# Optimization experiments

Measured on AMD Instinct MI355X. Metric: run time of the kernel, lower is better.

## Reference

```python
import jax, jax.numpy as jnp
import numpy as np

B, T, D = 4, 2048, 1024
H, K, V, S, C = 8, 128, 128, 512, 256
R = T // C
W = 2 * C
TAU = float(K) ** 0.5
NEG = 1e30  # INFTY_APPROX from source


def rel_shift(x):
    # Transformer-XL relative shift; x: [B,H,R,C,W]
    lead = x.shape[:-2]
    c, w = x.shape[-2:]
    x = jnp.pad(x, [(0, 0)] * (x.ndim - 1) + [(1, 0)])
    x = x.reshape(*lead, w + 1, c)
    return x[..., 1:, :].reshape(*lead, c, w)


def setup_inputs():
    key = jax.random.key(0)
    ks = jax.random.split(key, 9)
    sd = lambda n: 1.0 / np.sqrt(n)
    f32 = jnp.float32
    return dict(
        x=jax.random.normal(ks[0], (B, T, D), f32),
        g_ln=jnp.ones((D,), f32),
        Wq=jax.random.normal(ks[1], (D, H, K), f32) * sd(D),
        Wk=jax.random.normal(ks[2], (D, H, K), f32) * sd(D),
        Wv=jax.random.normal(ks[3], (D, H, V), f32) * sd(D),
        codebook=jax.random.normal(ks[4], (H, S, K), f32),
        xl_r=jax.random.normal(ks[5], (H, W, K), f32) * sd(D),
        xl_u=jax.random.normal(ks[6], (H, K), f32) * 0.02,
        xl_v=jax.random.normal(ks[7], (H, K), f32) * 0.02,
        Wo=jax.random.normal(ks[8], (H, V, D), f32) * sd(H * V),
    )


def reference(x, g_ln, Wq, Wk, Wv, codebook, xl_r, xl_u, xl_v, Wo):
    # RMSNorm
    xt = x * jax.lax.rsqrt(jnp.mean(jnp.square(x), axis=-1, keepdims=True) + 1e-6) * g_ln
    # QKV projections, reshaped to blocks: [B,H,R,C,*]
    q = jnp.einsum('btd,dhk->bhtk', xt, Wq).reshape(B, H, R, C, K)
    k = jnp.einsum('btd,dhk->bhtk', xt, Wk).reshape(B, H, R, C, K)
    v = jnp.einsum('btd,dhv->bhtv', xt, Wv).reshape(B, H, R, C, V)
    # VQ codebook assignment (per-head nearest codeword)
    d2 = (jnp.sum(k * k, -1, keepdims=True)
          - 2.0 * jnp.einsum('bhrck,hsk->bhrcs', k, codebook)
          + jnp.sum(codebook * codebook, -1)[None, :, None, None, :])
    z = jnp.argmin(d2, axis=-1)                      # shortcodes [B,H,R,C]
    delta = jax.nn.one_hot(z, S, dtype=k.dtype)      # [B,H,R,C,S]
    k_hat_q = jnp.einsum('bhrcs,hsk->bhrck', delta, codebook)
    k_hat = k + jax.lax.stop_gradient(k_hat_q - k)   # straight-through quantized keys
    # causal cumulative per-code cluster stats ('matmul' reduction from source)
    d1 = jnp.sum(delta, axis=3)                      # counts per block [B,H,R,S]
    d1c = jnp.cumsum(d1, axis=2)
    fracs = jnp.tril(jnp.einsum('bhrs,bhgs->bhsrg', 1.0 / jnp.clip(d1c, 1.0), d1))
    lower = jnp.pad(d1c[:, :, :-2], ((0, 0), (0, 0), (2, 0), (0, 0)))
    dv = jnp.einsum('bhrcs,bhrcv->bhrsv', delta, v)
    dvn = dv / jnp.clip(d1[..., None], 1.0)
    dvnc = jnp.einsum('bhsrg,bhgsv->bhrsv', fracs, dvn)
    upper_div_lower = jnp.pad(dvnc[:, :, :-2], ((0, 0), (0, 0), (2, 0), (0, 0), (0, 0)))
    # attention over recent window (prev+current block) and codebook cache
    q_u = q + xl_u[None, :, None, None, :]
    q_v = q + xl_v[None, :, None, None, :]
    k_hat_prev = jnp.pad(k_hat[:, :, :-1], ((0, 0), (0, 0), (1, 0), (0, 0), (0, 0)))
    v_prev = jnp.pad(v[:, :, :-1], ((0, 0), (0, 0), (1, 0), (0, 0), (0, 0)))
    k_recent = jnp.concatenate([k_hat_prev, k_hat], axis=3)  # [B,H,R,W,K]
    v_recent = jnp.concatenate([v_prev, v], axis=3)          # [B,H,R,W,V]
    ac = jnp.einsum('bhrck,bhrwk->bhrcw', q_u, k_recent)
    bd = rel_shift(jnp.einsum('bhrck,hwk->bhrcw', q_v, xl_r))
    recent = (ac + bd) / TAU
    i = jnp.arange(C)[:, None]
    j = jnp.arange(W)[None, :]
    causal = j <= i + C                                            # [C,W]
    first = (jnp.arange(R)[:, None, None] == 0) & (j[None] < C)    # mask zero-padded prev of block 0
    mask = causal[None] & jnp.logical_not(first)                   # [R,C,W]
    recent = jnp.where(mask[None, None], recent, -NEG)
    cache = jnp.einsum('bhrck,hsk->bhrcs', q_u, codebook) / TAU
    cache = cache + jnp.where(lower > 0, jnp.log(jnp.maximum(lower, 1.0)), -NEG)[:, :, :, None, :]
    attn = jax.nn.softmax(jnp.concatenate([cache, recent], axis=-1), axis=-1)
    out = (jnp.einsum('bhrcs,bhrsv->bhrcv', attn[..., :S], upper_div_lower)
           + jnp.einsum('bhrcw,bhrwv->bhrcv', attn[..., S:], v_recent))
    res = jnp.einsum('bhtv,hvd->btd', out.reshape(B, H, T, V), Wo)
    return res
```

## Files before the change

kernel.cpp:

```cpp
#include <hip/hip_runtime.h>
#include <hip/hip_fp16.h>

typedef _Float16 half8 __attribute__((ext_vector_type(8)));
typedef float f32x4 __attribute__((ext_vector_type(4)));

constexpr int Bn = 4, Tn = 2048, Dn = 1024, Hn = 8, Kn = 128, Vn = 128;
constexpr int Sn = 512, Cn = 256, Rn = 8, Wn = 512;
constexpr float NEGV = 1.0e30f;
constexpr float INV_TAU = 0.08838834764831845f;
constexpr int VTS = 74;

__device__ __forceinline__ half8 ldh8(const __half* p) {
  return *reinterpret_cast<const half8*>(p);
}
__device__ __forceinline__ void sth8(__half* p, half8 v) {
  *reinterpret_cast<half8*>(p) = v;
}
__device__ __forceinline__ f32x4 mfma16(half8 a, half8 b, f32x4 c) {
  return __builtin_amdgcn_mfma_f32_16x16x32_f16(a, b, c, 0, 0, 0);
}

__global__ __launch_bounds__(256) void rms3_k(const float* __restrict__ x,
                                              const float* __restrict__ g,
                                              __half* __restrict__ xth,
                                              __half* __restrict__ xtl) {
  const int row = blockIdx.x;
  const int tid = threadIdx.x;
  const float4 v = reinterpret_cast<const float4*>(x + (size_t)row * Dn)[tid];
  float ss = v.x * v.x + v.y * v.y + v.z * v.z + v.w * v.w;
#pragma unroll
  for (int o = 32; o > 0; o >>= 1) ss += __shfl_xor(ss, o);
  __shared__ float red[4];
  if ((tid & 63) == 0) red[tid >> 6] = ss;
  __syncthreads();
  const float tot = red[0] + red[1] + red[2] + red[3];
  const float sc = rsqrtf(tot * (1.0f / Dn) + 1e-6f);
  const float4 gv = reinterpret_cast<const float4*>(g)[tid];
  float vv[4] = {v.x * sc * gv.x, v.y * sc * gv.y, v.z * sc * gv.z,
                 v.w * sc * gv.w};
  __half hi[4], lo[4];
#pragma unroll
  for (int e = 0; e < 4; ++e) {
    hi[e] = __float2half(vv[e]);
    lo[e] = __float2half(vv[e] - __half2float(hi[e]));
  }
  __half2* oph = reinterpret_cast<__half2*>(xth + (size_t)row * Dn + tid * 4);
  __half2* opl = reinterpret_cast<__half2*>(xtl + (size_t)row * Dn + tid * 4);
  oph[0] = __halves2half2(hi[0], hi[1]);
  oph[1] = __halves2half2(hi[2], hi[3]);
  opl[0] = __halves2half2(lo[0], lo[1]);
  opl[1] = __halves2half2(lo[2], lo[3]);
}

__global__ __launch_bounds__(256) void transall_k(
    const float* __restrict__ Wq, const float* __restrict__ Wv,
    const float* __restrict__ Wo, const float* __restrict__ Wk,
    __half* __restrict__ wqt, __half* __restrict__ wvt,
    __half* __restrict__ wot, __half* __restrict__ wkth,
    __half* __restrict__ wktl) {
  __shared__ float ts[32][33];
  const int z = blockIdx.z;
  const float* src = (z == 0) ? Wq : (z == 1) ? Wv : (z == 2) ? Wo : Wk;
  const int bx = blockIdx.x, by = blockIdx.y;
  const int j = threadIdx.x & 31, i0 = threadIdx.x >> 5;
#pragma unroll
  for (int rr = 0; rr < 4; ++rr) {
    const int row = i0 + rr * 8;
    ts[row][j] = src[(size_t)(by * 32 + row) * 1024 + bx * 32 + j];
  }
  __syncthreads();
  if (z < 3) {
    __half* dst = (z == 0) ? wqt : (z == 1) ? wvt : wot;
#pragma unroll
    for (int rr = 0; rr < 4; ++rr) {
      const int row = i0 + rr * 8;
      dst[(size_t)(bx * 32 + row) * 1024 + by * 32 + j] =
          __float2half(ts[j][row]);
    }
  } else {
#pragma unroll
    for (int rr = 0; rr < 4; ++rr) {
      const int row = i0 + rr * 8;
      const float v = ts[j][row];
      const __half hi = __float2half(v);
      wkth[(size_t)(bx * 32 + row) * 1024 + by * 32 + j] = hi;
      wktl[(size_t)(bx * 32 + row) * 1024 + by * 32 + j] =
          __float2half(v - __half2float(hi));
    }
  }
}

__global__ __launch_bounds__(256) void cb2_k(const float* __restrict__ cb,
                                             float* __restrict__ cb2v) {
  const int idx = blockIdx.x * 256 + threadIdx.x;
  const float4* rp = reinterpret_cast<const float4*>(cb + (size_t)idx * Kn);
  float ss = 0.f;
#pragma unroll 8
  for (int i = 0; i < Kn / 4; ++i) {
    const float4 v = rp[i];
    ss += v.x * v.x + v.y * v.y + v.z * v.z + v.w * v.w;
  }
  cb2v[idx] = ss;
}

__global__ __launch_bounds__(256) void cvt2_k(const float* __restrict__ cb,
                                              const float* __restrict__ xlr,
                                              __half* __restrict__ cbh,
                                              __half* __restrict__ cbl,
                                              __half* __restrict__ xlrh) {
  const int i = blockIdx.x * 256 + threadIdx.x;
  constexpr int NE = Hn * Sn * Kn;
  if (i < NE) {
    const float v = cb[i];
    const __half hi = __float2half(v);
    cbh[i] = hi;
    cbl[i] = __float2half(v - __half2float(hi));
  } else {
    xlrh[i - NE] = __float2half(xlr[i - NE]);
  }
}

__global__ __launch_bounds__(256) void duv_k(const float* __restrict__ xlr,
                                             const float* __restrict__ xlu,
                                             const float* __restrict__ xlv,
                                             float* __restrict__ duv) {
  const int h = blockIdx.x;
  const float* up = xlu + h * Kn;
  const float* vp = xlv + h * Kn;
  for (int j = threadIdx.x; j < Wn; j += 256) {
    const float* rp = xlr + ((size_t)h * Wn + j) * Kn;
    float s = 0.f;
#pragma unroll 8
    for (int d = 0; d < Kn; ++d) s = fmaf(vp[d] - up[d], rp[d], s);
    duv[h * Wn + j] = s;
  }
}

__global__ __launch_bounds__(256, 2) void kproj_k(
    const __half* __restrict__ Ah, const __half* __restrict__ Al,
    const __half* __restrict__ Bh, const __half* __restrict__ Bl,
    __half* __restrict__ Ch, __half* __restrict__ Cl, int M, int KD) {
  __shared__ __half AsH[128 * 72];
  __shared__ __half AsL[128 * 72];
  __shared__ __half BsH[128 * 72];
  __shared__ __half BsL[128 * 72];
  const int tid = threadIdx.x;
  const int lane = tid & 63, wq = tid >> 6;
  const int lrow = lane & 15, lk8 = (lane >> 4) << 3;
  const int m0 = blockIdx.x * 128, n0 = blockIdx.y * 128;
  const int srow = tid >> 2, spart = tid & 3;

  f32x4 acc[2][8];
#pragma unroll
  for (int mt = 0; mt < 2; ++mt)
#pragma unroll
    for (int nt = 0; nt < 8; ++nt) acc[mt][nt] = (f32x4){0.f, 0.f, 0.f, 0.f};

  for (int kt = 0; kt < KD; kt += 64) {
    __syncthreads();
#pragma unroll
    for (int hh = 0; hh < 2; ++hh) {
      const int row = srow + hh * 64;
      const size_t ao = (size_t)(m0 + row) * KD + kt + spart * 16;
      const size_t bo = (size_t)(n0 + row) * KD + kt + spart * 16;
      sth8(&AsH[row * 72 + spart * 16], ldh8(Ah + ao));
      sth8(&AsH[row * 72 + spart * 16 + 8], ldh8(Ah + ao + 8));
      sth8(&AsL[row * 72 + spart * 16], ldh8(Al + ao));
      sth8(&AsL[row * 72 + spart * 16 + 8], ldh8(Al + ao + 8));
      sth8(&BsH[row * 72 + spart * 16], ldh8(Bh + bo));
      sth8(&BsH[row * 72 + spart * 16 + 8], ldh8(Bh + bo + 8));
      sth8(&BsL[row * 72 + spart * 16], ldh8(Bl + bo));
      sth8(&BsL[row * 72 + spart * 16 + 8], ldh8(Bl + bo + 8));
    }
    __syncthreads();
#pragma unroll
    for (int ks = 0; ks < 2; ++ks) {
      const half8 a0h = ldh8(&AsH[(32 * wq + lrow) * 72 + lk8 + 32 * ks]);
      const half8 a1h = ldh8(&AsH[(32 * wq + 16 + lrow) * 72 + lk8 + 32 * ks]);
      const half8 a0l = ldh8(&AsL[(32 * wq + lrow) * 72 + lk8 + 32 * ks]);
      const half8 a1l = ldh8(&AsL[(32 * wq + 16 + lrow) * 72 + lk8 + 32 * ks]);
#pragma unroll
      for (int nt = 0; nt < 8; ++nt) {
        const half8 bh = ldh8(&BsH[(16 * nt + lrow) * 72 + lk8 + 32 * ks]);
        const half8 bl = ldh8(&BsL[(16 * nt + lrow) * 72 + lk8 + 32 * ks]);
        acc[0][nt] = mfma16(a0h, bh, acc[0][nt]);
        acc[0][nt] = mfma16(a0h, bl, acc[0][nt]);
        acc[0][nt] = mfma16(a0l, bh, acc[0][nt]);
        acc[1][nt] = mfma16(a1h, bh, acc[1][nt]);
        acc[1][nt] = mfma16(a1h, bl, acc[1][nt]);
        acc[1][nt] = mfma16(a1l, bh, acc[1][nt]);
      }
    }
  }
  __half* OH = Ch + (size_t)(n0 >> 7) * M * 128;
  __half* OL = Cl + (size_t)(n0 >> 7) * M * 128;
#pragma unroll
  for (int mt = 0; mt < 2; ++mt)
#pragma unroll
    for (int nt = 0; nt < 8; ++nt)
#pragma unroll
      for (int reg = 0; reg < 4; ++reg) {
        const int row = m0 + 32 * wq + 16 * mt + 4 * (lane >> 4) + reg;
        const float v = acc[mt][nt][reg];
        const __half hi = __float2half(v);
        OH[(size_t)row * 128 + 16 * nt + lrow] = hi;
        OL[(size_t)row * 128 + 16 * nt + lrow] =
            __float2half(v - __half2float(hi));
      }
}

template <int MODE>
__global__ __launch_bounds__(256, 4) void gemmh_k(const __half* __restrict__ A,
                                                  const __half* __restrict__ Bt,
                                                  void* __restrict__ Cout,
                                                  int M, int N, int KD) {
  __shared__ __half As[128 * 72];
  __shared__ __half Bs[128 * 72];
  const int tid = threadIdx.x;
  const int lane = tid & 63, wq = tid >> 6;
  const int lrow = lane & 15, lk8 = (lane >> 4) << 3;
  const int m0 = blockIdx.x * 128, n0 = blockIdx.y * 128;
  const int srow = tid >> 2, spart = tid & 3;

  f32x4 acc[2][8];
#pragma unroll
  for (int mt = 0; mt < 2; ++mt)
#pragma unroll
    for (int nt = 0; nt < 8; ++nt) acc[mt][nt] = (f32x4){0.f, 0.f, 0.f, 0.f};

  for (int kt = 0; kt < KD; kt += 64) {
    __syncthreads();
#pragma unroll
    for (int hh = 0; hh < 2; ++hh) {
      const int row = srow + hh * 64;
      const __half* pa = A + (size_t)(m0 + row) * KD + kt + spart * 16;
      const __half* pb = Bt + (size_t)(n0 + row) * KD + kt + spart * 16;
      sth8(&As[row * 72 + spart * 16], ldh8(pa));
      sth8(&As[row * 72 + spart * 16 + 8], ldh8(pa + 8));
      sth8(&Bs[row * 72 + spart * 16], ldh8(pb));
      sth8(&Bs[row * 72 + spart * 16 + 8], ldh8(pb + 8));
    }
    __syncthreads();
#pragma unroll
    for (int ks = 0; ks < 2; ++ks) {
      half8 a0 = ldh8(&As[(32 * wq + lrow) * 72 + lk8 + 32 * ks]);
      half8 a1 = ldh8(&As[(32 * wq + 16 + lrow) * 72 + lk8 + 32 * ks]);
#pragma unroll
      for (int nt = 0; nt < 8; ++nt) {
        half8 b = ldh8(&Bs[(16 * nt + lrow) * 72 + lk8 + 32 * ks]);
        acc[0][nt] = mfma16(a0, b, acc[0][nt]);
        acc[1][nt] = mfma16(a1, b, acc[1][nt]);
      }
    }
  }
  if (MODE == 0) {
    __half* O = reinterpret_cast<__half*>(Cout) + (size_t)(n0 >> 7) * M * 128;
#pragma unroll
    for (int mt = 0; mt < 2; ++mt)
#pragma unroll
      for (int nt = 0; nt < 8; ++nt)
#pragma unroll
        for (int reg = 0; reg < 4; ++reg) {
          const int row = m0 + 32 * wq + 16 * mt + 4 * (lane >> 4) + reg;
          O[(size_t)row * 128 + 16 * nt + lrow] = __float2half(acc[mt][nt][reg]);
        }
  } else {
    float* O = reinterpret_cast<float*>(Cout);
#pragma unroll
    for (int mt = 0; mt < 2; ++mt)
#pragma unroll
      for (int nt = 0; nt < 8; ++nt)
#pragma unroll
        for (int reg = 0; reg < 4; ++reg) {
          const int row = m0 + 32 * wq + 16 * mt + 4 * (lane >> 4) + reg;
          O[(size_t)row * N + n0 + 16 * nt + lrow] = acc[mt][nt][reg];
        }
  }
}

__global__ __launch_bounds__(256, 2) void argmin3_k(
    const __half* __restrict__ kbh, const __half* __restrict__ kbl,
    const __half* __restrict__ cbh, const __half* __restrict__ cbl,
    const float* __restrict__ cb2v, int* __restrict__ zb) {
  __shared__ __half BsH[64 * 136];
  __shared__ __half BsL[64 * 136];
  const int tid = threadIdx.x;
  const int lane = tid & 63, wq = tid >> 6;
  const int lrow = lane & 15, lk8 = (lane >> 4) << 3;
  const int m0 = blockIdx.x * 128;
  const int h = blockIdx.y;
  const int srow = tid >> 2, spart = tid & 3;
  const size_t kbase = (size_t)h * (Bn * Tn);

  half8 ah[2][4], al[2][4];
#pragma unroll
  for (int mt = 0; mt < 2; ++mt)
#pragma unroll
    for (int ks = 0; ks < 4; ++ks) {
      const size_t off =
          (kbase + m0 + 32 * wq + 16 * mt + lrow) * 128 + lk8 + 32 * ks;
      ah[mt][ks] = ldh8(kbh + off);
      al[mt][ks] = ldh8(kbl + off);
    }

  float best[2][4];
  int bidx[2][4];
#pragma unroll
  for (int mt = 0; mt < 2; ++mt)
#pragma unroll
    for (int reg = 0; reg < 4; ++reg) {
      best[mt][reg] = 3.0e38f;
      bidx[mt][reg] = 0;
    }

  for (int s0 = 0; s0 < Sn; s0 += 64) {
    __syncthreads();
    {
      const size_t bo = ((size_t)h * Sn + s0 + srow) * 128 + spart * 32;
      sth8(&BsH[srow * 136 + spart * 32], ldh8(cbh + bo));
      sth8(&BsH[srow * 136 + spart * 32 + 8], ldh8(cbh + bo + 8));
      sth8(&BsH[srow * 136 + spart * 32 + 16], ldh8(cbh + bo + 16));
      sth8(&BsH[srow * 136 + spart * 32 + 24], ldh8(cbh + bo + 24));
      sth8(&BsL[srow * 136 + spart * 32], ldh8(cbl + bo));
      sth8(&BsL[srow * 136 + spart * 32 + 8], ldh8(cbl + bo + 8));
      sth8(&BsL[srow * 136 + spart * 32 + 16], ldh8(cbl + bo + 16));
      sth8(&BsL[srow * 136 + spart * 32 + 24], ldh8(cbl + bo + 24));
    }
    __syncthreads();
    f32x4 acc[2][4];
#pragma unroll
    for (int mt = 0; mt < 2; ++mt)
#pragma unroll
      for (int nt = 0; nt < 4; ++nt) acc[mt][nt] = (f32x4){0.f, 0.f, 0.f, 0.f};
#pragma unroll
    for (int ks = 0; ks < 4; ++ks)
#pragma unroll
      for (int nt = 0; nt < 4; ++nt) {
        const half8 bh = ldh8(&BsH[(16 * nt + lrow) * 136 + lk8 + 32 * ks]);
        const half8 bl = ldh8(&BsL[(16 * nt + lrow) * 136 + lk8 + 32 * ks]);
        acc[0][nt] = mfma16(ah[0][ks], bh, acc[0][nt]);
        acc[0][nt] = mfma16(ah[0][ks], bl, acc[0][nt]);
        acc[0][nt] = mfma16(al[0][ks], bh, acc[0][nt]);
        acc[1][nt] = mfma16(ah[1][ks], bh, acc[1][nt]);
        acc[1][nt] = mfma16(ah[1][ks], bl, acc[1][nt]);
        acc[1][nt] = mfma16(al[1][ks], bh, acc[1][nt]);
      }
#pragma unroll
    for (int mt = 0; mt < 2; ++mt)
#pragma unroll
      for (int nt = 0; nt < 4; ++nt) {
        const int s = s0 + 16 * nt + lrow;
        const float c2 = cb2v[h * Sn + s];
#pragma unroll
        for (int reg = 0; reg < 4; ++reg) {
          const float d2 = c2 - 2.0f * acc[mt][nt][reg];
          if (d2 < best[mt][reg]) {
            best[mt][reg] = d2;
            bidx[mt][reg] = s;
          }
        }
      }
  }
#pragma unroll
  for (int xb = 1; xb <= 8; xb <<= 1) {
#pragma unroll
    for (int mt = 0; mt < 2; ++mt)
#pragma unroll
      for (int reg = 0; reg < 4; ++reg) {
        const float ob = __shfl_xor(best[mt][reg], xb);
        const int oi = __shfl_xor(bidx[mt][reg], xb);
        if (ob < best[mt][reg] ||
            (ob == best[mt][reg] && oi < bidx[mt][reg])) {
          best[mt][reg] = ob;
          bidx[mt][reg] = oi;
        }
      }
  }
  if (lrow == 0) {
#pragma unroll
    for (int mt = 0; mt < 2; ++mt)
#pragma unroll
      for (int reg = 0; reg < 4; ++reg) {
        const int row = m0 + 32 * wq + 16 * mt + 4 * (lane >> 4) + reg;
        zb[kbase + row] = bidx[mt][reg];
      }
  }
}

__global__ __launch_bounds__(1024) void scan2_k(const int* __restrict__ zb,
                                                const __half* __restrict__ vb,
                                                __half* __restrict__ udl,
                                                float* __restrict__ biasv) {
  __shared__ float acc[64][128];
  __shared__ float cnt[64];
  const int tid = threadIdx.x;
  const int sc = blockIdx.x, b = blockIdx.y, h = blockIdx.z;
  const int s0 = sc * 64;
  for (int i = tid; i < 64 * 128; i += 1024) acc[i >> 7][i & 127] = 0.f;
  if (tid < 64) cnt[tid] = 0.f;
  __syncthreads();
  const size_t tokH = (size_t)h * (Bn * Tn) + (size_t)b * Tn;
  const int dd = tid & 127, slice = tid >> 7;
  for (int r = 0; r < Rn; ++r) {
    for (int i = tid; i < 64 * 128; i += 1024) {
      const int srow = i >> 7, d = i & 127;
      const float c = cnt[srow];
      udl[((((size_t)h * Bn + b) * Rn + r) * Sn + s0 + srow) * Vn + d] =
          __float2half(acc[srow][d] / fmaxf(c, 1.f));
    }
    if (tid < 64) {
      const float c = cnt[tid];
      biasv[(((size_t)h * Bn + b) * Rn + r) * Sn + s0 + tid] =
          (c > 0.f) ? logf(c) : -NEGV;
    }
    __syncthreads();
    if (r >= 1 && r < 7) {
      const int tb = (r - 1) * Cn;
#pragma unroll 4
      for (int u = 0; u < 32; ++u) {
        const int tok = tb + u * 8 + slice;
        const int s = zb[tokH + tok];
        if (s >= s0 && s < s0 + 64) {
          const float v = __half2float(vb[(tokH + tok) * Vn + dd]);
          atomicAdd(&acc[s - s0][dd], v);
          if (dd == 0) atomicAdd(&cnt[s - s0], 1.0f);
        }
      }
    }
    __syncthreads();
  }
}

__global__ __launch_bounds__(512, 2) void attn7_k(
    const __half* __restrict__ qbh, const __half* __restrict__ vbh,
    const __half* __restrict__ udl, const __half* __restrict__ cbh,
    const __half* __restrict__ xlrh, const float* __restrict__ biasv,
    const float* __restrict__ duv, const int* __restrict__ zb,
    const float* __restrict__ xlu, __half* __restrict__ aout) {
  __shared__ __half XS[320 * 136];
  __shared__ __half KS[64 * 136];
  __shared__ __half VtS[128 * VTS];
  __shared__ __half Ebuf[8 * 16 * 82];

  const int tid = threadIdx.x;
  const int lane = tid & 63, wq = tid >> 6;
  const int lrow = lane & 15, hi = lane >> 4, lk8 = hi << 3;
  const int bx = blockIdx.x;
  const int b = bx >> 3, r = bx & 7;
  const int h = blockIdx.y;
  const int cm0 = 32 * wq;
  const size_t tokH = (size_t)h * (Bn * Tn) + (size_t)b * Tn;
  const size_t sBase = (((size_t)h * Bn + b) * Rn + r) * Sn;
  const int tBlk = r * Cn;
  __half* Ew = &Ebuf[wq * 16 * 82];
  __half* Pw = &XS[(40 * wq) * 136];

  half8 a[2][4];
#pragma unroll
  for (int mt = 0; mt < 2; ++mt) {
    const size_t qrow = (tokH + tBlk + cm0 + 16 * mt + lrow) * Kn;
#pragma unroll
    for (int ks = 0; ks < 4; ++ks) {
      const int col = lk8 + 32 * ks;
      half8 q = ldh8(qbh + qrow + col);
      const float* up = xlu + h * Kn + col;
      half8 t;
#pragma unroll
      for (int e = 0; e < 8; ++e) t[e] = (_Float16)((float)q[e] + up[e]);
      a[mt][ks] = t;
    }
  }

  float mR[2][4], lR[2][4];
  f32x4 Oacc[2][8];
#pragma unroll
  for (int mt = 0; mt < 2; ++mt) {
#pragma unroll
    for (int i = 0; i < 4; ++i) {
      mR[mt][i] = -NEGV;
      lR[mt][i] = 0.f;
    }
#pragma unroll
    for (int nt = 0; nt < 8; ++nt) Oacc[mt][nt] = (f32x4){0.f, 0.f, 0.f, 0.f};
  }

  const int krow = tid >> 3, kpart = tid & 7;
  const int kp = tid >> 4, p16 = tid & 15;

  const int chStart = (r >= 2) ? 0 : ((r == 1) ? 8 : 12);

  for (int ch = chStart; ch < 16; ++ch) {
    const bool isC = (ch < 8);
    const int s0 = ch * 64;
    const int w0 = (ch - 8) * 64;
    __syncthreads();
    if (isC) {
      {
        const __half* ks = cbh + ((size_t)h * Sn + s0 + krow) * Kn + kpart * 16;
        sth8(&KS[krow * 136 + kpart * 16], ldh8(ks));
        sth8(&KS[krow * 136 + kpart * 16 + 8], ldh8(ks + 8));
      }
      {
        const __half* u0 = udl + (sBase + s0 + 2 * kp) * Vn + p16 * 8;
        const __half* u1 = u0 + Vn;
#pragma unroll
        for (int e = 0; e < 8; ++e) {
          const int d = p16 * 8 + e;
          const int gidx = ((2 * kp) >> 3) ^ ((d >> 4) & 7);
          *reinterpret_cast<__half2*>(
              &VtS[d * VTS + gidx * 8 + ((2 * kp) & 7)]) =
              __halves2half2(u0[e], u1[e]);
        }
      }
    } else {
      {
        int tk = (r - 1) * Cn + w0 + krow;
        if (tk < 0) tk = 0;
        const int code = zb[tokH + tk];
        const __half* ks = cbh + ((size_t)h * Sn + code) * Kn + kpart * 16;
        sth8(&KS[krow * 136 + kpart * 16], ldh8(ks));
        sth8(&KS[krow * 136 + kpart * 16 + 8], ldh8(ks + 8));
      }
      {
        const int tk0 = (r - 1) * Cn + w0 + 2 * kp;
        const int tka = tk0 < 0 ? 0 : tk0;
        const int tkb = tk0 + 1 < 0 ? 0 : tk0 + 1;
        const __half* v0 = vbh + (tokH + tka) * Kn + p16 * 8;
        const __half* v1 = vbh + (tokH + tkb) * Kn + p16 * 8;
#pragma unroll
        for (int e = 0; e < 8; ++e) {
          const int d = p16 * 8 + e;
          const int gidx = ((2 * kp) >> 3) ^ ((d >> 4) & 7);
          *reinterpret_cast<__half2*>(
              &VtS[d * VTS + gidx * 8 + ((2 * kp) & 7)]) =
              __halves2half2(v0[e], v1[e]);
        }
      }
      for (int jl = tid >> 1; jl < 320; jl += 256) {
        const int p2 = tid & 1;
        int j = w0 + jl;
        j = j > Wn - 1 ? Wn - 1 : j;
        const __half* xs = xlrh + ((size_t)h * Wn + j) * Kn + 64 * p2;
        __half* xd = &XS[jl * 136 + 64 * p2];
#pragma unroll
        for (int g8 = 0; g8 < 8; ++g8) sth8(xd + 8 * g8, ldh8(xs + 8 * g8));
      }
    }
    __syncthreads();

    f32x4 acc[2][4];
#pragma unroll
    for (int mt = 0; mt < 2; ++mt)
#pragma unroll
      for (int nt = 0; nt < 4; ++nt) acc[mt][nt] = (f32x4){0.f, 0.f, 0.f, 0.f};
#pragma unroll
    for (int ks = 0; ks < 4; ++ks) {
#pragma unroll
      for (int nt = 0; nt < 4; ++nt) {
        const half8 bfr = ldh8(&KS[(16 * nt + lrow) * 136 + lk8 + 32 * ks]);
        acc[0][nt] = mfma16(a[0][ks], bfr, acc[0][nt]);
        acc[1][nt] = mfma16(a[1][ks], bfr, acc[1][nt]);
      }
    }

    float lg[2][4][4];
    if (isC) {
#pragma unroll
      for (int nt = 0; nt < 4; ++nt) {
        const float bv = biasv[sBase + s0 + 16 * nt + lrow];
#pragma unroll
        for (int mt = 0; mt < 2; ++mt)
#pragma unroll
          for (int reg = 0; reg < 4; ++reg)
            lg[mt][nt][reg] = acc[mt][nt][reg] * INV_TAU + bv;
      }
    } else {
#pragma unroll
      for (int mt = 0; mt < 2; ++mt) {
        const int cmt = cm0 + 16 * mt;
        const int bbase = 240 - cmt;
        f32x4 eacc[5];
#pragma unroll
        for (int nt = 0; nt < 5; ++nt) eacc[nt] = (f32x4){0.f, 0.f, 0.f, 0.f};
#pragma unroll
        for (int ks = 0; ks < 4; ++ks)
#pragma unroll
          for (int nt = 0; nt < 5; ++nt)
            eacc[nt] = mfma16(
                a[mt][ks],
                ldh8(&XS[(bbase + 16 * nt + lrow) * 136 + lk8 + 32 * ks]),
                eacc[nt]);
#pragma unroll
        for (int nt = 0; nt < 5; ++nt) {
          int j = w0 + bbase + 16 * nt + lrow;
          j = j > Wn - 1 ? Wn - 1 : j;
          const float dv = duv[h * Wn + j];
#pragma unroll
          for (int reg = 0; reg < 4; ++reg)
            Ew[(4 * hi + reg) * 82 + 16 * nt + lrow] =
                __float2half(eacc[nt][reg] + dv);
        }
#pragma unroll
        for (int nt = 0; nt < 4; ++nt) {
          const int kw = 16 * nt + lrow;
          const int w = w0 + kw;
#pragma unroll
          for (int reg = 0; reg < 4; ++reg) {
            const int cl = 4 * hi + reg;
            const int cabs = cmt + cl;
            const bool valid = (w <= cabs + Cn) && !(r == 0 && w < Cn);
            const float bdv = __half2float(Ew[cl * 82 + kw + 15 - cl]);
            lg[mt][nt][reg] =
                valid ? (acc[mt][nt][reg] + bdv) * INV_TAU : -NEGV;
          }
        }
      }
    }
    float p[2][4][4];
#pragma unroll
    for (int mt = 0; mt < 2; ++mt) {
#pragma unroll
      for (int reg = 0; reg < 4; ++reg) {
        float rm = fmaxf(fmaxf(lg[mt][0][reg], lg[mt][1][reg]),
                         fmaxf(lg[mt][2][reg], lg[mt][3][reg]));
        rm = fmaxf(rm, __shfl_xor(rm, 1));
        rm = fmaxf(rm, __shfl_xor(rm, 2));
        rm = fmaxf(rm, __shfl_xor(rm, 4));
        rm = fmaxf(rm, __shfl_xor(rm, 8));
        const float mn = fmaxf(mR[mt][reg], rm);
        const float scl = __expf(mR[mt][reg] - mn);
        float rs = 0.f;
#pragma unroll
        for (int nt = 0; nt < 4; ++nt) {
          p[mt][nt][reg] = __expf(lg[mt][nt][reg] - mn);
          rs += p[mt][nt][reg];
        }
        rs += __shfl_xor(rs, 1);
        rs += __shfl_xor(rs, 2);
        rs += __shfl_xor(rs, 4);
        rs += __shfl_xor(rs, 8);
        lR[mt][reg] = lR[mt][reg] * scl + rs;
        mR[mt][reg] = mn;
#pragma unroll
        for (int nt = 0; nt < 8; ++nt) Oacc[mt][nt][reg] *= scl;
      }
    }
    if (!isC) __syncthreads();
#pragma unroll
    for (int mt = 0; mt < 2; ++mt)
#pragma unroll
      for (int nt = 0; nt < 4; ++nt)
#pragma unroll
        for (int reg = 0; reg < 4; ++reg)
          Pw[(16 * mt + 4 * hi + reg) * 136 + lrow + 16 * nt] =
              __float2half(p[mt][nt][reg]);
#pragma unroll
    for (int ks = 0; ks < 2; ++ks) {
#pragma unroll
      for (int mt = 0; mt < 2; ++mt) {
        const half8 pa = ldh8(&Pw[(16 * mt + lrow) * 136 + lk8 + 32 * ks]);
#pragma unroll
        for (int nt = 0; nt < 8; ++nt) {
          const int gidx = (((lk8 + 32 * ks) >> 3) ^ nt);
          const half8 vv = ldh8(&VtS[(16 * nt + lrow) * VTS + gidx * 8]);
          Oacc[mt][nt] = mfma16(pa, vv, Oacc[mt][nt]);
        }
      }
    }
  }
#pragma unroll
  for (int mt = 0; mt < 2; ++mt) {
    float inv[4];
#pragma unroll
    for (int reg = 0; reg < 4; ++reg) inv[reg] = 1.0f / lR[mt][reg];
#pragma unroll
    for (int nt = 0; nt < 8; ++nt)
#pragma unroll
      for (int reg = 0; reg < 4; ++reg) {
        const int c = cm0 + 16 * mt + 4 * hi + reg;
        aout[((size_t)b * Tn + tBlk + c) * (Hn * Vn) + h * Vn + 16 * nt +
             lrow] = __float2half(Oacc[mt][nt][reg] * inv[reg]);
      }
  }
}

extern "C" void kernel_launch(void* const* d_in, const int* in_sizes, int n_in,
                              void* d_out, int out_size, void* d_ws,
                              size_t ws_size, hipStream_t stream) {
  (void)in_sizes;
  (void)n_in;
  (void)out_size;
  const float* x = (const float*)d_in[0];
  const float* g_ln = (const float*)d_in[1];
  const float* Wq = (const float*)d_in[2];
  const float* Wk = (const float*)d_in[3];
  const float* Wv = (const float*)d_in[4];
  const float* cb = (const float*)d_in[5];
  const float* xl_r = (const float*)d_in[6];
  const float* xl_u = (const float*)d_in[7];
  const float* xl_v = (const float*)d_in[8];
  const float* Wo = (const float*)d_in[9];
  float* out = (float*)d_out;

  float* W = (float*)d_ws;
  size_t o = 0;
  __half* xth = (__half*)(W + o);
  __half* aout = xth;
  o += (size_t)Bn * Tn * Dn / 2;
  __half* xtl = (__half*)(W + o);
  o += (size_t)Bn * Tn * Dn / 2;
  __half* kbh = (__half*)(W + o);
  __half* udlh = kbh;
  o += (size_t)Hn * Bn * Tn * Kn / 2;
  __half* kbl = (__half*)(W + o);
  o += (size_t)Hn * Bn * Tn * Kn / 2;
  __half* qbh = (__half*)(W + o);
  o += (size_t)Hn * Bn * Tn * Kn / 2;
  __half* vbh = (__half*)(W + o);
  o += (size_t)Hn * Bn * Tn * Vn / 2;
  __half* cbh = (__half*)(W + o);
  o += (size_t)Hn * Sn * Kn / 2;
  __half* cbl = (__half*)(W + o);
  o += (size_t)Hn * Sn * Kn / 2;
  __half* xlrh = (__half*)(W + o);
  o += (size_t)Hn * Wn * Kn / 2;
  int* zb = (int*)(W + o);
  o += (size_t)Hn * Bn * Tn;
  float* biasb = W + o;
  o += (size_t)Hn * Bn * Rn * Sn;
  float* duvb = W + o;
  o += (size_t)Hn * Wn;
  float* cb2b = W + o;
  o += (size_t)Hn * Sn;
  __half* wkth = (__half*)(W + o);
  o += (size_t)Dn * Dn / 2;
  __half* wktl = (__half*)(W + o);
  o += (size_t)Dn * Dn / 2;
  __half* wqt = (__half*)(W + o);
  o += (size_t)Dn * Dn / 2;
  __half* wvt = (__half*)(W + o);
  o += (size_t)Dn * Dn / 2;
  __half* wot = (__half*)(W + o);
  o += (size_t)Dn * Dn / 2;

  if (ws_size < o * sizeof(float)) return;

  rms3_k<<<Bn * Tn, 256, 0, stream>>>(x, g_ln, xth, xtl);
  transall_k<<<dim3(32, 32, 4), 256, 0, stream>>>(Wq, Wv, Wo, Wk, wqt, wvt,
                                                  wot, wkth, wktl);
  cb2_k<<<Hn * Sn / 256, 256, 0, stream>>>(cb, cb2b);
  cvt2_k<<<2 * Hn * Sn * Kn / 256, 256, 0, stream>>>(cb, xl_r, cbh, cbl, xlrh);
  duv_k<<<Hn, 256, 0, stream>>>(xl_r, xl_u, xl_v, duvb);

  kproj_k<<<dim3(64, 8), 256, 0, stream>>>(xth, xtl, wkth, wktl, kbh, kbl,
                                           8192, 1024);
  gemmh_k<0><<<dim3(64, 8), 256, 0, stream>>>(xth, wqt, qbh, 8192, 1024, 1024);
  gemmh_k<0><<<dim3(64, 8), 256, 0, stream>>>(xth, wvt, vbh, 8192, 1024, 1024);

  argmin3_k<<<dim3(Bn * Tn / 128, Hn), 256, 0, stream>>>(kbh, kbl, cbh, cbl,
                                                         cb2b, zb);
  scan2_k<<<dim3(8, Bn, Hn), 1024, 0, stream>>>(zb, vbh, udlh, biasb);

  attn7_k<<<dim3(Bn * Rn, Hn), 512, 0, stream>>>(
      qbh, vbh, udlh, cbh, xlrh, biasb, duvb, zb, xl_u, aout);

  gemmh_k<1><<<dim3(64, 8), 256, 0, stream>>>(aout, wot, out, 8192, 1024,
                                              1024);
}
```

Measured before the change: 438.0 us.

## Reuse xl_r window across recent chunks via ring buffer and drop extra barrier

The 320-row xl_r window in shared memory becomes a circular buffer. It is loaded in full only on the first recent chunk, and each later chunk loads just the 64 new rows instead of reloading all 320. The P staging area moves out of XS into a separate per-warp scratch region shared with the E buffer, which lets the extra __syncthreads before the P writes be removed. The V-transpose row stride also changes from 74 to 72, which could reintroduce LDS bank conflicts.

New measurement: 393.2 us. 10.2% less time.

```diff
diff --git a/kernel.cpp b/kernel.cpp
--- a/kernel.cpp
+++ b/kernel.cpp
@@ -8,7 +8,6 @@
 constexpr int Sn = 512, Cn = 256, Rn = 8, Wn = 512;
 constexpr float NEGV = 1.0e30f;
 constexpr float INV_TAU = 0.08838834764831845f;
-constexpr int VTS = 74;
 
 __device__ __forceinline__ half8 ldh8(const __half* p) {
   return *reinterpret_cast<const half8*>(p);
@@ -431,7 +430,7 @@
   }
 }
 
-__global__ __launch_bounds__(512, 2) void attn7_k(
+__global__ __launch_bounds__(512, 2) void attn8_k(
     const __half* __restrict__ qbh, const __half* __restrict__ vbh,
     const __half* __restrict__ udl, const __half* __restrict__ cbh,
     const __half* __restrict__ xlrh, const float* __restrict__ biasv,
@@ -439,8 +438,8 @@
     const float* __restrict__ xlu, __half* __restrict__ aout) {
   __shared__ __half XS[320 * 136];
   __shared__ __half KS[64 * 136];
-  __shared__ __half VtS[128 * VTS];
-  __shared__ __half Ebuf[8 * 16 * 82];
+  __shared__ __half VtS[128 * 72];
+  __shared__ __half SC[8 * 2304];
 
   const int tid = threadIdx.x;
   const int lane = tid & 63, wq = tid >> 6;
@@ -452,8 +451,7 @@
   const size_t tokH = (size_t)h * (Bn * Tn) + (size_t)b * Tn;
   const size_t sBase = (((size_t)h * Bn + b) * Rn + r) * Sn;
   const int tBlk = r * Cn;
-  __half* Ew = &Ebuf[wq * 16 * 82];
-  __half* Pw = &XS[(40 * wq) * 136];
+  __half* Sw = &SC[wq * 2304];
 
   half8 a[2][4];
 #pragma unroll
@@ -488,11 +486,13 @@
   const int kp = tid >> 4, p16 = tid & 15;
 
   const int chStart = (r >= 2) ? 0 : ((r == 1) ? 8 : 12);
+  const int chFirstRecent = (chStart > 8) ? chStart : 8;
 
   for (int ch = chStart; ch < 16; ++ch) {
     const bool isC = (ch < 8);
     const int s0 = ch * 64;
     const int w0 = (ch - 8) * 64;
+    const int w0m = (w0 >= 320) ? w0 - 320 : w0;
     __syncthreads();
     if (isC) {
       {
@@ -508,7 +508,7 @@
           const int d = p16 * 8 + e;
           const int gidx = ((2 * kp) >> 3) ^ ((d >> 4) & 7);
           *reinterpret_cast<__half2*>(
-              &VtS[d * VTS + gidx * 8 + ((2 * kp) & 7)]) =
+              &VtS[d * 72 + gidx * 8 + ((2 * kp) & 7)]) =
               __halves2half2(u0[e], u1[e]);
         }
       }
@@ -532,18 +532,32 @@
           const int d = p16 * 8 + e;
           const int gidx = ((2 * kp) >> 3) ^ ((d >> 4) & 7);
           *reinterpret_cast<__half2*>(
-              &VtS[d * VTS + gidx * 8 + ((2 * kp) & 7)]) =
+              &VtS[d * 72 + gidx * 8 + ((2 * kp) & 7)]) =
               __halves2half2(v0[e], v1[e]);
         }
       }
-      for (int jl = tid >> 1; jl < 320; jl += 256) {
-        const int p2 = tid & 1;
+      if (ch == chFirstRecent) {
+        for (int jl = tid >> 1; jl < 320; jl += 256) {
+          const int p2 = tid & 1;
+          int j = w0 + jl;
+          j = j > Wn - 1 ? Wn - 1 : j;
+          int pos = w0m + jl;
+          if (pos >= 320) pos -= 320;
+          const __half* xs = xlrh + ((size_t)h * Wn + j) * Kn + 64 * p2;
+          __half* xd = &XS[pos * 136 + 64 * p2];
+#pragma unroll
+          for (int g8 = 0; g8 < 8; ++g8) sth8(xd + 8 * g8, ldh8(xs + 8 * g8));
+        }
+      } else {
+        const int jl = 256 + (tid >> 3);
         int j = w0 + jl;
         j = j > Wn - 1 ? Wn - 1 : j;
-        const __half* xs = xlrh + ((size_t)h * Wn + j) * Kn + 64 * p2;
-        __half* xd = &XS[jl * 136 + 64 * p2];
-#pragma unroll
-        for (int g8 = 0; g8 < 8; ++g8) sth8(xd + 8 * g8, ldh8(xs + 8 * g8));
+        int pos = w0m + jl;
+        if (pos >= 320) pos -= 320;
+        const __half* xs = xlrh + ((size_t)h * Wn + j) * Kn + (tid & 7) * 16;
+        __half* xd = &XS[pos * 136 + (tid & 7) * 16];
+        sth8(xd, ldh8(xs));
+        sth8(xd + 8, ldh8(xs + 8));
       }
     }
     __syncthreads();
@@ -579,6 +593,14 @@
       for (int mt = 0; mt < 2; ++mt) {
         const int cmt = cm0 + 16 * mt;
         const int bbase = 240 - cmt;
+        const int posB = w0m + bbase;
+        int xrow[5];
+#pragma unroll
+        for (int nt = 0; nt < 5; ++nt) {
+          int rr = posB + 16 * nt + lrow;
+          if (rr >= 320) rr -= 320;
+          xrow[nt] = rr;
+        }
         f32x4 eacc[5];
 #pragma unroll
         for (int nt = 0; nt < 5; ++nt) eacc[nt] = (f32x4){0.f, 0.f, 0.f, 0.f};
@@ -586,10 +608,9 @@
         for (int ks = 0; ks < 4; ++ks)
 #pragma unroll
           for (int nt = 0; nt < 5; ++nt)
-            eacc[nt] = mfma16(
-                a[mt][ks],
-                ldh8(&XS[(bbase + 16 * nt + lrow) * 136 + lk8 + 32 * ks]),
-                eacc[nt]);
+            eacc[nt] = mfma16(a[mt][ks],
+                              ldh8(&XS[xrow[nt] * 136 + lk8 + 32 * ks]),
+                              eacc[nt]);
 #pragma unroll
         for (int nt = 0; nt < 5; ++nt) {
           int j = w0 + bbase + 16 * nt + lrow;
@@ -597,7 +618,7 @@
           const float dv = duv[h * Wn + j];
 #pragma unroll
           for (int reg = 0; reg < 4; ++reg)
-            Ew[(4 * hi + reg) * 82 + 16 * nt + lrow] =
+            Sw[(4 * hi + reg) * 82 + 16 * nt + lrow] =
                 __float2half(eacc[nt][reg] + dv);
         }
 #pragma unroll
@@ -609,7 +630,7 @@
             const int cl = 4 * hi + reg;
             const int cabs = cmt + cl;
             const bool valid = (w <= cabs + Cn) && !(r == 0 && w < Cn);
-            const float bdv = __half2float(Ew[cl * 82 + kw + 15 - cl]);
+            const float bdv = __half2float(Sw[cl * 82 + kw + 15 - cl]);
             lg[mt][nt][reg] =
                 valid ? (acc[mt][nt][reg] + bdv) * INV_TAU : -NEGV;
           }
@@ -645,24 +666,23 @@
         for (int nt = 0; nt < 8; ++nt) Oacc[mt][nt][reg] *= scl;
       }
     }
-    if (!isC) __syncthreads();
 #pragma unroll
     for (int mt = 0; mt < 2; ++mt)
 #pragma unroll
       for (int nt = 0; nt < 4; ++nt)
 #pragma unroll
         for (int reg = 0; reg < 4; ++reg)
-          Pw[(16 * mt + 4 * hi + reg) * 136 + lrow + 16 * nt] =
+          Sw[(16 * mt + 4 * hi + reg) * 72 + lrow + 16 * nt] =
               __float2half(p[mt][nt][reg]);
 #pragma unroll
     for (int ks = 0; ks < 2; ++ks) {
 #pragma unroll
       for (int mt = 0; mt < 2; ++mt) {
-        const half8 pa = ldh8(&Pw[(16 * mt + lrow) * 136 + lk8 + 32 * ks]);
+        const half8 pa = ldh8(&Sw[(16 * mt + lrow) * 72 + lk8 + 32 * ks]);
 #pragma unroll
         for (int nt = 0; nt < 8; ++nt) {
           const int gidx = (((lk8 + 32 * ks) >> 3) ^ nt);
-          const half8 vv = ldh8(&VtS[(16 * nt + lrow) * VTS + gidx * 8]);
+          const half8 vv = ldh8(&VtS[(16 * nt + lrow) * 72 + gidx * 8]);
           Oacc[mt][nt] = mfma16(pa, vv, Oacc[mt][nt]);
         }
       }
@@ -761,7 +781,7 @@
                                                          cb2b, zb);
   scan2_k<<<dim3(8, Bn, Hn), 1024, 0, stream>>>(zb, vbh, udlh, biasb);
 
-  attn7_k<<<dim3(Bn * Rn, Hn), 512, 0, stream>>>(
+  attn8_k<<<dim3(Bn * Rn, Hn), 512, 0, stream>>>(
       qbh, vbh, udlh, cbh, xlrh, biasb, duvb, zb, xl_u, aout);
 
   gemmh_k<1><<<dim3(64, 8), 256, 0, stream>>>(aout, wot, out, 8192, 1024,
```
